# Kernel optimization log

Hardware: AMD Instinct MI355X
Metric: run time of the kernel (lower is better)

The kernel has to match this reference:

```python
import jax, jax.numpy as jnp
import numpy as np

SCALE = 0.02
EPS = 1e-5


def setup_inputs() -> dict:
    key = jax.random.key(0)
    ks = jax.random.split(key, 11)
    C = 256
    inp = {
        "x": jax.random.normal(ks[0], (64, C, 28, 28), dtype=jnp.float32),
        "w1": jax.random.normal(ks[1], (C, C, 3, 3), dtype=jnp.float32) * 0.05,
        "g1": jax.random.uniform(ks[2], (C,), dtype=jnp.float32, minval=0.5, maxval=1.5),
        "b1": jax.random.normal(ks[3], (C,), dtype=jnp.float32) * 0.1,
        "m1": jax.random.normal(ks[4], (C,), dtype=jnp.float32) * 0.1,
        "v1": jax.random.uniform(ks[5], (C,), dtype=jnp.float32, minval=0.5, maxval=1.5),
        "w2": jax.random.normal(ks[6], (C, C, 3, 3), dtype=jnp.float32) * 0.05,
        "g2": jax.random.uniform(ks[7], (C,), dtype=jnp.float32, minval=0.5, maxval=1.5),
        "b2": jax.random.normal(ks[8], (C,), dtype=jnp.float32) * 0.1,
        "m2": jax.random.normal(ks[9], (C,), dtype=jnp.float32) * 0.1,
        "v2": jax.random.uniform(ks[10], (C,), dtype=jnp.float32, minval=0.5, maxval=1.5),
    }
    return inp


def _bin_conv3x3(x, w, stride=1):
    # 1-bit weight conv: sign(w)*scale, straight-through estimator for grads.
    wb = w + jax.lax.stop_gradient(jnp.sign(w) - w)
    y = jax.lax.conv_general_dilated(
        x, wb,
        window_strides=(stride, stride),
        padding=[(1, 1), (1, 1)],
        dimension_numbers=("NCHW", "OIHW", "NCHW"),
    )
    return y * SCALE


def _bn(x, g, b, m, v):
    # eval-mode batchnorm with running stats
    inv = g * jax.lax.rsqrt(v + EPS)  # [C]
    return x * inv[None, :, None, None] + (b - m * inv)[None, :, None, None]


def reference(x, w1, g1, b1, m1, v1, w2, g2, b2, m2, v2):
    out = jax.nn.relu(_bn(_bin_conv3x3(x, w1, 1), g1, b1, m1, v1))
    out = _bn(_bin_conv3x3(out, w2, 1), g2, b2, m2, v2)
    return jax.nn.relu(out + x)
```

## Files before the change

### kernel.cpp

```cpp
#include <hip/hip_runtime.h>

#define N_IMG 64
#define C_CH 256
#define PADW 30
#define SPIMG 784
#define PADIMG 900
#define SCALE_F 0.02f
#define EPS_F 1e-5f

using short8  = __attribute__((ext_vector_type(8))) short;
using floatx4 = __attribute__((ext_vector_type(4))) float;

__device__ __forceinline__ unsigned short f2bf(float f) {
  unsigned u = __float_as_uint(f);
  return (unsigned short)((u + 0x7fffu + ((u >> 16) & 1u)) >> 16);
}


__global__ void pack_weights(const float* __restrict__ w1, const float* __restrict__ w2,
                             unsigned short* __restrict__ ap1, unsigned short* __restrict__ ap2) {
  int t = blockIdx.x * 256 + threadIdx.x;
  const float* __restrict__ w = blockIdx.y ? w2 : w1;
  unsigned short* __restrict__ ap = blockIdx.y ? ap2 : ap1;
  float v = w[t];
  int off = t % 9;
  int ct  = t / 9;
  int ci  = ct & 255;
  int co  = ct >> 8;
  unsigned short b = (v > 0.f) ? 0x3F80u : ((v < 0.f) ? 0xBF80u : 0u);
  ap[((off * 32 + (ci >> 3)) * 256 + co) * 8 + (ci & 7)] = b;
}

__global__ void bn_prep(const float* g1, const float* b1, const float* m1, const float* v1,
                        const float* g2, const float* b2, const float* m2, const float* v2,
                        float* bnp) {
  int c = threadIdx.x;
  float inv1 = g1[c] * rsqrtf(v1[c] + EPS_F);
  bnp[c]       = SCALE_F * inv1;
  bnp[256 + c] = b1[c] - m1[c] * inv1;
  float inv2 = g2[c] * rsqrtf(v2[c] + EPS_F);
  bnp[512 + c] = SCALE_F * inv2;
  bnp[768 + c] = b2[c] - m2[c] * inv2;
}

__global__ void convert_x(const float* __restrict__ x, unsigned short* __restrict__ xb) {
  __shared__ float tile[28 * 260];
  int h = blockIdx.x;
  int n = blockIdx.y;
  int tid = threadIdx.x;
  const float* xs = x + ((size_t)n * C_CH) * SPIMG + h * 28;
  for (int u = tid; u < 1792; u += 256) {
    int ci = u / 7;
    int w4 = u - ci * 7;
    floatx4 f = *(const floatx4*)&xs[(size_t)ci * SPIMG + w4 * 4];
    tile[(w4 * 4 + 0) * 260 + ci] = f[0];
    tile[(w4 * 4 + 1) * 260 + ci] = f[1];
    tile[(w4 * 4 + 2) * 260 + ci] = f[2];
    tile[(w4 * 4 + 3) * 260 + ci] = f[3];
  }
  __syncthreads();
  unsigned short* xd = xb + ((size_t)n * PADIMG + (h + 1) * PADW + 1) * C_CH;
  for (int u = tid; u < 1792; u += 256) {
    int w  = u >> 6;
    int c4 = u & 63;
    floatx4 f = *(const floatx4*)&tile[w * 260 + c4 * 4];
    ushort4 o;
    o.x = f2bf(f[0]); o.y = f2bf(f[1]); o.z = f2bf(f[2]); o.w = f2bf(f[3]);
    *(ushort4*)(xd + (size_t)w * C_CH + c4 * 4) = o;
  }
}

__global__ void zero_borders(unsigned short* __restrict__ xb, unsigned short* __restrict__ abuf) {
  int n = blockIdx.x;
  unsigned short* b = (blockIdx.y ? abuf : xb) + (size_t)n * PADIMG * C_CH;
  for (int u = threadIdx.x; u < 7424; u += 256) {
    int px = u >> 6, c4 = u & 63;
    int h, w;
    if (px < 30)      { h = 0;       w = px;      }
    else if (px < 60) { h = 29;      w = px - 30; }
    else if (px < 88) { h = px - 59; w = 0;       }
    else              { h = px - 87; w = 29;      }
    ushort4 z = {0, 0, 0, 0};
    *(ushort4*)(b + (size_t)(h * PADW + w) * C_CH + c4 * 4) = z;
  }
}

template<int STAGE>
__global__ __launch_bounds__(256, 2) void bconv(
    const unsigned short* __restrict__ Bin,
    const unsigned short* __restrict__ Apack,
    const float* __restrict__ bnp,
    unsigned short* __restrict__ aout,
    const float* __restrict__ xres,
    float* __restrict__ out)
{
  __shared__ __align__(16) unsigned short Blds[180 * 72];

  const int tid  = threadIdx.x;
  const int lane = tid & 63;
  const int wv   = tid >> 6;
  const int quad = lane >> 4;
  const int l16  = lane & 15;
  const int spBlk = blockIdx.x;
  const int n     = blockIdx.y;

  const int prow0 = 4 * spBlk;
  const unsigned short* bsrc = Bin + (size_t)n * PADIMG * C_CH + (size_t)(prow0 * PADW) * C_CH;
  const int coW = wv * 64;

  int bOff[7];
#pragma unroll
  for (int s = 0; s < 7; ++s) {
    int lm = s * 16 + l16;
    int hl = lm / 28;
    int w  = lm - hl * 28;
    bOff[s] = (hl * 30 + w) * 72 + quad * 8;
  }

  floatx4 acc[4][7];
#pragma unroll
  for (int c = 0; c < 4; ++c)
#pragma unroll
    for (int s = 0; s < 7; ++s)
      acc[c][s] = (floatx4){0.f, 0.f, 0.f, 0.f};

#pragma unroll 1
  for (int cib = 0; cib < 256; cib += 64) {
    __syncthreads();
    for (int u = tid; u < 1440; u += 256) {
      int px = u >> 3, c8 = (u & 7) * 8;
      const unsigned short* src = bsrc + (size_t)px * C_CH + cib + c8;
      *(short8*)&Blds[px * 72 + c8] = *(const short8*)src;
    }
    __syncthreads();

    const int cbase = (cib >> 3) + quad;
#pragma unroll 1
    for (int kh = 0; kh < 3; ++kh) {
#pragma unroll 1
      for (int kw = 0; kw < 3; ++kw) {
        const int doff72 = (kh * 30 + kw) * 72;
        const int chunkB = (kh * 3 + kw) * 32 + cbase;
#pragma unroll
        for (int half = 0; half < 2; ++half) {
          const int chunk = chunkB + half * 4;
          const unsigned short* apb = Apack + ((size_t)chunk * 256 + coW + l16) * 8;
          short8 a0 = *(const short8*)(apb);
          short8 a1 = *(const short8*)(apb + 16 * 8);
          short8 a2 = *(const short8*)(apb + 32 * 8);
          short8 a3 = *(const short8*)(apb + 48 * 8);
          const int bo = doff72 + half * 32;
#pragma unroll
          for (int s = 0; s < 7; ++s) {
            short8 b = *(const short8*)&Blds[bOff[s] + bo];
            acc[0][s] = __builtin_amdgcn_mfma_f32_16x16x32_bf16(a0, b, acc[0][s], 0, 0, 0);
            acc[1][s] = __builtin_amdgcn_mfma_f32_16x16x32_bf16(a1, b, acc[1][s], 0, 0, 0);
            acc[2][s] = __builtin_amdgcn_mfma_f32_16x16x32_bf16(a2, b, acc[2][s], 0, 0, 0);
            acc[3][s] = __builtin_amdgcn_mfma_f32_16x16x32_bf16(a3, b, acc[3][s], 0, 0, 0);
          }
        }
      }
    }
  }

  if (STAGE == 1) {
#pragma unroll
    for (int c = 0; c < 4; ++c) {
      int co = coW + c * 16 + quad * 4;
      floatx4 As = *(const floatx4*)(bnp + co);
      floatx4 Bs = *(const floatx4*)(bnp + 256 + co);
#pragma unroll
      for (int s = 0; s < 7; ++s) {
        int lm = s * 16 + l16;
        int hl = lm / 28;
        int w  = lm - hl * 28;
        int pix = (prow0 + hl + 1) * PADW + w + 1;
        unsigned short* dst = aout + ((size_t)n * PADIMG + pix) * C_CH + co;
        ushort4 o;
        o.x = f2bf(fmaxf(acc[c][s][0] * As[0] + Bs[0], 0.f));
        o.y = f2bf(fmaxf(acc[c][s][1] * As[1] + Bs[1], 0.f));
        o.z = f2bf(fmaxf(acc[c][s][2] * As[2] + Bs[2], 0.f));
        o.w = f2bf(fmaxf(acc[c][s][3] * As[3] + Bs[3], 0.f));
        *(ushort4*)dst = o;
      }
    }
  } else {
#pragma unroll
    for (int c = 0; c < 4; ++c) {
      int co = coW + c * 16 + quad * 4;
      floatx4 As = *(const floatx4*)(bnp + 512 + co);
      floatx4 Bs = *(const floatx4*)(bnp + 768 + co);
#pragma unroll
      for (int s = 0; s < 7; ++s) {
        int m = spBlk * 112 + s * 16 + l16;
#pragma unroll
        for (int r = 0; r < 4; ++r) {
          size_t oidx = ((size_t)n * C_CH + co + r) * SPIMG + m;
          float v = acc[c][s][r] * As[r] + Bs[r] + xres[oidx];
          out[oidx] = fmaxf(v, 0.f);
        }
      }
    }
  }
}


extern "C" void kernel_launch(void* const* d_in, const int* in_sizes, int n_in,
                              void* d_out, int out_size, void* d_ws, size_t ws_size,
                              hipStream_t stream) {
  const float* x  = (const float*)d_in[0];
  const float* w1 = (const float*)d_in[1];
  const float* g1 = (const float*)d_in[2];
  const float* b1 = (const float*)d_in[3];
  const float* m1 = (const float*)d_in[4];
  const float* v1 = (const float*)d_in[5];
  const float* w2 = (const float*)d_in[6];
  const float* g2 = (const float*)d_in[7];
  const float* b2 = (const float*)d_in[8];
  const float* m2 = (const float*)d_in[9];
  const float* v2 = (const float*)d_in[10];
  float* out = (float*)d_out;

  char* ws = (char*)d_ws;
  const size_t PADBUF = (size_t)N_IMG * PADIMG * C_CH * 2;
  const size_t WPACK  = 589824ull * 2;
  unsigned short* xb   = (unsigned short*)ws;
  unsigned short* abuf = (unsigned short*)(ws + PADBUF);
  unsigned short* ap1  = (unsigned short*)(ws + 2 * PADBUF);
  unsigned short* ap2  = (unsigned short*)(ws + 2 * PADBUF + WPACK);
  float* bnp           = (float*)(ws + 2 * PADBUF + 2 * WPACK);

  zero_borders<<<dim3(N_IMG, 2), 256, 0, stream>>>(xb, abuf);
  pack_weights<<<dim3(2304, 2), 256, 0, stream>>>(w1, w2, ap1, ap2);
  bn_prep<<<1, 256, 0, stream>>>(g1, b1, m1, v1, g2, b2, m2, v2, bnp);
  convert_x<<<dim3(28, N_IMG), 256, 0, stream>>>(x, xb);

  dim3 grid(7, N_IMG);
  bconv<1><<<grid, 256, 0, stream>>>(xb,   ap1, bnp, abuf, nullptr, nullptr);
  bconv<2><<<grid, 256, 0, stream>>>(abuf, ap2, bnp, nullptr, x, out);
}
```

Before: 273.8 us.

## Double-buffer LDS with async global-to-LDS loads and software-pipelined MFMA fragments

The conv kernel now double-buffers the activation tile in LDS and fills it with direct global_load_lds transfers issued mid-loop for the next channel block. The LDS layout is XOR-swizzled without padding to avoid bank conflicts. A and B fragments are register double-buffered across the 18 tap/half steps so loads overlap MFMAs. Separately, the prep kernels are merged (weight pack + BN prep, x conversion + border zeroing) to cut launches. This raises LDS and register use, which could lower occupancy.

```diff
diff --git a/kernel.cpp b/kernel.cpp
--- a/kernel.cpp
+++ b/kernel.cpp
@@ -1,12 +1,7 @@
 #include <hip/hip_runtime.h>
 
-#define N_IMG 64
-#define C_CH 256
-#define PADW 30
-#define SPIMG 784
-#define PADIMG 900
+#define EPS_F 1e-5f
 #define SCALE_F 0.02f
-#define EPS_F 1e-5f
 
 using short8  = __attribute__((ext_vector_type(8))) short;
 using floatx4 = __attribute__((ext_vector_type(4))) float;
@@ -16,9 +11,17 @@
   return (unsigned short)((u + 0x7fffu + ((u >> 16) & 1u)) >> 16);
 }
 
-
-__global__ void pack_weights(const float* __restrict__ w1, const float* __restrict__ w2,
-                             unsigned short* __restrict__ ap1, unsigned short* __restrict__ ap2) {
+__device__ __forceinline__ void gl_lds16(const unsigned short* g, unsigned short* l) {
+  __builtin_amdgcn_global_load_lds(
+      (const __attribute__((address_space(1))) unsigned int*)g,
+      (__attribute__((address_space(3))) unsigned int*)l, 16, 0, 0);
+}
+
+__global__ void prep_w(const float* __restrict__ w1, const float* __restrict__ w2,
+                       unsigned short* __restrict__ ap1, unsigned short* __restrict__ ap2,
+                       const float* g1, const float* b1, const float* m1, const float* v1,
+                       const float* g2, const float* b2, const float* m2, const float* v2,
+                       float* bnp) {
   int t = blockIdx.x * 256 + threadIdx.x;
   const float* __restrict__ w = blockIdx.y ? w2 : w1;
   unsigned short* __restrict__ ap = blockIdx.y ? ap2 : ap1;
@@ -29,59 +32,79 @@
   int co  = ct >> 8;
   unsigned short b = (v > 0.f) ? 0x3F80u : ((v < 0.f) ? 0xBF80u : 0u);
   ap[((off * 32 + (ci >> 3)) * 256 + co) * 8 + (ci & 7)] = b;
-}
-
-__global__ void bn_prep(const float* g1, const float* b1, const float* m1, const float* v1,
-                        const float* g2, const float* b2, const float* m2, const float* v2,
-                        float* bnp) {
-  int c = threadIdx.x;
-  float inv1 = g1[c] * rsqrtf(v1[c] + EPS_F);
-  bnp[c]       = SCALE_F * inv1;
-  bnp[256 + c] = b1[c] - m1[c] * inv1;
-  float inv2 = g2[c] * rsqrtf(v2[c] + EPS_F);
-  bnp[512 + c] = SCALE_F * inv2;
-  bnp[768 + c] = b2[c] - m2[c] * inv2;
-}
-
-__global__ void convert_x(const float* __restrict__ x, unsigned short* __restrict__ xb) {
+  if (blockIdx.x == 0 && blockIdx.y == 0) {
+    int c = threadIdx.x;
+    float i1 = g1[c] * rsqrtf(v1[c] + EPS_F);
+    bnp[c]       = SCALE_F * i1;
+    bnp[256 + c] = b1[c] - m1[c] * i1;
+    float i2 = g2[c] * rsqrtf(v2[c] + EPS_F);
+    bnp[512 + c] = SCALE_F * i2;
+    bnp[768 + c] = b2[c] - m2[c] * i2;
+  }
+}
+
+__global__ void prep_x(const float* __restrict__ x, unsigned short* __restrict__ xb,
+                       unsigned short* __restrict__ abuf) {
   __shared__ float tile[28 * 260];
   int h = blockIdx.x;
   int n = blockIdx.y;
   int tid = threadIdx.x;
-  const float* xs = x + ((size_t)n * C_CH) * SPIMG + h * 28;
+  const float* xs = x + ((size_t)n * 256) * 784 + h * 28;
   for (int u = tid; u < 1792; u += 256) {
     int ci = u / 7;
-    int w4 = u - ci * 7;
-    floatx4 f = *(const floatx4*)&xs[(size_t)ci * SPIMG + w4 * 4];
-    tile[(w4 * 4 + 0) * 260 + ci] = f[0];
-    tile[(w4 * 4 + 1) * 260 + ci] = f[1];
-    tile[(w4 * 4 + 2) * 260 + ci] = f[2];
-    tile[(w4 * 4 + 3) * 260 + ci] = f[3];
+    int j  = u - ci * 7;
+    floatx4 f = *(const floatx4*)&xs[(size_t)ci * 784 + j * 4];
+    tile[(j * 4 + 0) * 260 + ci] = f[0];
+    tile[(j * 4 + 1) * 260 + ci] = f[1];
+    tile[(j * 4 + 2) * 260 + ci] = f[2];
+    tile[(j * 4 + 3) * 260 + ci] = f[3];
   }
   __syncthreads();
-  unsigned short* xd = xb + ((size_t)n * PADIMG + (h + 1) * PADW + 1) * C_CH;
+  unsigned short* xd = xb + ((size_t)n * 900 + (h + 1) * 30 + 1) * 256;
   for (int u = tid; u < 1792; u += 256) {
     int w  = u >> 6;
     int c4 = u & 63;
     floatx4 f = *(const floatx4*)&tile[w * 260 + c4 * 4];
     ushort4 o;
     o.x = f2bf(f[0]); o.y = f2bf(f[1]); o.z = f2bf(f[2]); o.w = f2bf(f[3]);
-    *(ushort4*)(xd + (size_t)w * C_CH + c4 * 4) = o;
-  }
-}
-
-__global__ void zero_borders(unsigned short* __restrict__ xb, unsigned short* __restrict__ abuf) {
-  int n = blockIdx.x;
-  unsigned short* b = (blockIdx.y ? abuf : xb) + (size_t)n * PADIMG * C_CH;
-  for (int u = threadIdx.x; u < 7424; u += 256) {
-    int px = u >> 6, c4 = u & 63;
-    int h, w;
-    if (px < 30)      { h = 0;       w = px;      }
-    else if (px < 60) { h = 29;      w = px - 30; }
-    else if (px < 88) { h = px - 59; w = 0;       }
-    else              { h = px - 87; w = 29;      }
+    *(ushort4*)(xd + (size_t)w * 256 + c4 * 4) = o;
+  }
+  {
+    int bufi = tid >> 7, side = (tid >> 6) & 1, c4 = tid & 63;
+    unsigned short* bb = (bufi ? abuf : xb) + ((size_t)n * 900 + (h + 1) * 30 + side * 29) * 256;
     ushort4 z = {0, 0, 0, 0};
-    *(ushort4*)(b + (size_t)(h * PADW + w) * C_CH + c4 * 4) = z;
+    *(ushort4*)(bb + c4 * 4) = z;
+  }
+  if (h == 0 || h == 27) {
+    int row = (h == 0) ? 0 : 29;
+    for (int u = tid; u < 3840; u += 256) {
+      int bufi = u / 1920;
+      int r    = u - bufi * 1920;
+      int px   = r >> 6, c4 = r & 63;
+      unsigned short* bb = (bufi ? abuf : xb) + ((size_t)n * 900 + row * 30 + px) * 256;
+      ushort4 z = {0, 0, 0, 0};
+      *(ushort4*)(bb + c4 * 4) = z;
+    }
+  }
+}
+
+__device__ __forceinline__ void loadA4(short8* dst, const unsigned short* __restrict__ Apack,
+                                       int cib, int off, int half, int quad, int coW, int l16) {
+  int chunk = off * 32 + cib * 8 + half * 4 + quad;
+  const unsigned short* apb = Apack + ((size_t)(chunk * 256 + coW + l16)) * 8;
+#pragma unroll
+  for (int c = 0; c < 4; ++c) dst[c] = *(const short8*)(apb + c * 128);
+}
+
+__device__ __forceinline__ void loadB7(short8* dst, const unsigned short* Bl,
+                                       const int* pxS, int off, int half, int quad) {
+  const int D = (off / 3) * 30 + (off % 3);
+  const int C = half * 4 + quad;
+#pragma unroll
+  for (int s = 0; s < 7; ++s) {
+    int pe  = pxS[s] + D;
+    int idx = (pe << 6) + ((C ^ (pe & 7)) << 3);
+    dst[s] = *(const short8*)(Bl + idx);
   }
 }
 
@@ -94,7 +117,7 @@
     const float* __restrict__ xres,
     float* __restrict__ out)
 {
-  __shared__ __align__(16) unsigned short Blds[180 * 72];
+  __shared__ __align__(16) unsigned short Blds[2][192 * 64];
 
   const int tid  = threadIdx.x;
   const int lane = tid & 63;
@@ -105,17 +128,20 @@
   const int n     = blockIdx.y;
 
   const int prow0 = 4 * spBlk;
-  const unsigned short* bsrc = Bin + (size_t)n * PADIMG * C_CH + (size_t)(prow0 * PADW) * C_CH;
+  const unsigned short* bsrc = Bin + ((size_t)n * 900 + prow0 * 30) * 256;
   const int coW = wv * 64;
 
-  int bOff[7];
+  int pxS[7];
 #pragma unroll
   for (int s = 0; s < 7; ++s) {
     int lm = s * 16 + l16;
     int hl = lm / 28;
     int w  = lm - hl * 28;
-    bOff[s] = (hl * 30 + w) * 72 + quad * 8;
-  }
+    pxS[s] = hl * 30 + w;
+  }
+
+  const int sl_px = lane >> 3;
+  const int sl_ch = (lane & 7) ^ sl_px;
 
   floatx4 acc[4][7];
 #pragma unroll
@@ -124,43 +150,50 @@
     for (int s = 0; s < 7; ++s)
       acc[c][s] = (floatx4){0.f, 0.f, 0.f, 0.f};
 
+  short8 Af[2][4], Bf[2][7];
+  loadA4(Af[0], Apack, 0, 0, 0, quad, coW, l16);
+#pragma unroll
+  for (int i = 0; i < 6; ++i) {
+    int px0 = wv * 48 + i * 8;
+    int px = px0 + sl_px; px = px > 179 ? 179 : px;
+    gl_lds16(bsrc + (size_t)px * 256 + sl_ch * 8, &Blds[0][px0 * 64]);
+  }
+  __syncthreads();
+
+  int cur = 0;
 #pragma unroll 1
-  for (int cib = 0; cib < 256; cib += 64) {
+  for (int cib = 0; cib < 4; ++cib) {
+    const unsigned short* Bl = &Blds[cur][0];
+    loadB7(Bf[0], Bl, pxS, 0, 0, quad);
+#pragma unroll
+    for (int st = 0; st < 18; ++st) {
+      const int cu = st & 1, nx = cu ^ 1;
+      if (st < 17) {
+        const int o2 = (st + 1) >> 1, h2 = (st + 1) & 1;
+        loadA4(Af[nx], Apack, cib, o2, h2, quad, coW, l16);
+        loadB7(Bf[nx], Bl, pxS, o2, h2, quad);
+      }
+      if (st == 8 && cib < 3) {
+        const int ci0 = (cib + 1) * 64;
+        unsigned short* dbuf = &Blds[cur ^ 1][0];
+#pragma unroll
+        for (int i = 0; i < 6; ++i) {
+          int px0 = wv * 48 + i * 8;
+          int px = px0 + sl_px; px = px > 179 ? 179 : px;
+          gl_lds16(bsrc + (size_t)px * 256 + ci0 + sl_ch * 8, dbuf + px0 * 64);
+        }
+      }
+      if (st == 17 && cib < 3) {
+        loadA4(Af[nx], Apack, cib + 1, 0, 0, quad, coW, l16);
+      }
+#pragma unroll
+      for (int s = 0; s < 7; ++s)
+#pragma unroll
+        for (int c = 0; c < 4; ++c)
+          acc[c][s] = __builtin_amdgcn_mfma_f32_16x16x32_bf16(Af[cu][c], Bf[cu][s], acc[c][s], 0, 0, 0);
+    }
     __syncthreads();
-    for (int u = tid; u < 1440; u += 256) {
-      int px = u >> 3, c8 = (u & 7) * 8;
-      const unsigned short* src = bsrc + (size_t)px * C_CH + cib + c8;
-      *(short8*)&Blds[px * 72 + c8] = *(const short8*)src;
-    }
-    __syncthreads();
-
-    const int cbase = (cib >> 3) + quad;
-#pragma unroll 1
-    for (int kh = 0; kh < 3; ++kh) {
-#pragma unroll 1
-      for (int kw = 0; kw < 3; ++kw) {
-        const int doff72 = (kh * 30 + kw) * 72;
-        const int chunkB = (kh * 3 + kw) * 32 + cbase;
-#pragma unroll
-        for (int half = 0; half < 2; ++half) {
-          const int chunk = chunkB + half * 4;
-          const unsigned short* apb = Apack + ((size_t)chunk * 256 + coW + l16) * 8;
-          short8 a0 = *(const short8*)(apb);
-          short8 a1 = *(const short8*)(apb + 16 * 8);
-          short8 a2 = *(const short8*)(apb + 32 * 8);
-          short8 a3 = *(const short8*)(apb + 48 * 8);
-          const int bo = doff72 + half * 32;
-#pragma unroll
-          for (int s = 0; s < 7; ++s) {
-            short8 b = *(const short8*)&Blds[bOff[s] + bo];
-            acc[0][s] = __builtin_amdgcn_mfma_f32_16x16x32_bf16(a0, b, acc[0][s], 0, 0, 0);
-            acc[1][s] = __builtin_amdgcn_mfma_f32_16x16x32_bf16(a1, b, acc[1][s], 0, 0, 0);
-            acc[2][s] = __builtin_amdgcn_mfma_f32_16x16x32_bf16(a2, b, acc[2][s], 0, 0, 0);
-            acc[3][s] = __builtin_amdgcn_mfma_f32_16x16x32_bf16(a3, b, acc[3][s], 0, 0, 0);
-          }
-        }
-      }
-    }
+    cur ^= 1;
   }
 
   if (STAGE == 1) {
@@ -174,8 +207,8 @@
         int lm = s * 16 + l16;
         int hl = lm / 28;
         int w  = lm - hl * 28;
-        int pix = (prow0 + hl + 1) * PADW + w + 1;
-        unsigned short* dst = aout + ((size_t)n * PADIMG + pix) * C_CH + co;
+        int pix = (prow0 + hl + 1) * 30 + w + 1;
+        unsigned short* dst = aout + ((size_t)n * 900 + pix) * 256 + co;
         ushort4 o;
         o.x = f2bf(fmaxf(acc[c][s][0] * As[0] + Bs[0], 0.f));
         o.y = f2bf(fmaxf(acc[c][s][1] * As[1] + Bs[1], 0.f));
@@ -195,7 +228,7 @@
         int m = spBlk * 112 + s * 16 + l16;
 #pragma unroll
         for (int r = 0; r < 4; ++r) {
-          size_t oidx = ((size_t)n * C_CH + co + r) * SPIMG + m;
+          size_t oidx = ((size_t)n * 256 + co + r) * 784 + m;
           float v = acc[c][s][r] * As[r] + Bs[r] + xres[oidx];
           out[oidx] = fmaxf(v, 0.f);
         }
@@ -222,7 +255,7 @@
   float* out = (float*)d_out;
 
   char* ws = (char*)d_ws;
-  const size_t PADBUF = (size_t)N_IMG * PADIMG * C_CH * 2;
+  const size_t PADBUF = (size_t)64 * 900 * 256 * 2;
   const size_t WPACK  = 589824ull * 2;
   unsigned short* xb   = (unsigned short*)ws;
   unsigned short* abuf = (unsigned short*)(ws + PADBUF);
@@ -230,12 +263,11 @@
   unsigned short* ap2  = (unsigned short*)(ws + 2 * PADBUF + WPACK);
   float* bnp           = (float*)(ws + 2 * PADBUF + 2 * WPACK);
 
-  zero_borders<<<dim3(N_IMG, 2), 256, 0, stream>>>(xb, abuf);
-  pack_weights<<<dim3(2304, 2), 256, 0, stream>>>(w1, w2, ap1, ap2);
-  bn_prep<<<1, 256, 0, stream>>>(g1, b1, m1, v1, g2, b2, m2, v2, bnp);
-  convert_x<<<dim3(28, N_IMG), 256, 0, stream>>>(x, xb);
-
-  dim3 grid(7, N_IMG);
+  prep_w<<<dim3(2304, 2), 256, 0, stream>>>(w1, w2, ap1, ap2,
+                                            g1, b1, m1, v1, g2, b2, m2, v2, bnp);
+  prep_x<<<dim3(28, 64), 256, 0, stream>>>(x, xb, abuf);
+
+  dim3 grid(7, 64);
   bconv<1><<<grid, 256, 0, stream>>>(xb,   ap1, bnp, abuf, nullptr, nullptr);
   bconv<2><<<grid, 256, 0, stream>>>(abuf, ap2, bnp, nullptr, x, out);
 }
```

New measurement: 449.6 us. 1.64x slower.
